# Performance work log

Hardware: AMD Instinct MI355X
Metric: run time of the kernel (lower is better)

Reference implementation:

```python
import jax, jax.numpy as jnp
import numpy as np

B, S, D = 16, 1024, 512
H, DH = 8, 64  # heads, dim_head


def setup_inputs() -> dict:
    key = jax.random.key(0)
    ks = jax.random.split(key, 7)
    x = jax.random.normal(ks[0], (B, S, D), dtype=jnp.float32)
    # variable sequence lengths in [1, S]
    seq_lens = jnp.maximum(jax.random.randint(ks[1], (B,), 0, S + 1), 1).astype(jnp.int32)
    w_std = 0.02
    Wq = jax.random.normal(ks[2], (D, D), dtype=jnp.float32) * w_std
    Wk = jax.random.normal(ks[3], (D, D), dtype=jnp.float32) * w_std
    Wv = jax.random.normal(ks[4], (D, D), dtype=jnp.float32) * w_std
    Wo = jax.random.normal(ks[5], (D, D), dtype=jnp.float32) * w_std
    bo = jnp.zeros((D,), dtype=jnp.float32)
    return {"x": x, "seq_lens": seq_lens, "Wq": Wq, "Wk": Wk, "Wv": Wv, "Wo": Wo, "bo": bo}


def reference(x, seq_lens, Wq, Wk, Wv, Wo, bo):
    # x: [B, S, D] padded ragged batch; seq_lens: [B] valid token counts.
    # Equivalent to the per-batch SDPA loop over jagged sequences: attention
    # is computed only among the valid tokens of each sequence.
    scale = DH ** -0.5
    q = (x @ Wq).reshape(B, S, H, DH)
    k = (x @ Wk).reshape(B, S, H, DH)
    v = (x @ Wv).reshape(B, S, H, DH)
    scores = jnp.einsum('bqhd,bkhd->bhqk', q, k) * scale  # [B,H,S,S]
    valid = jnp.arange(S)[None, :] < seq_lens[:, None]     # [B,S] token mask
    neg_inf = jnp.finfo(scores.dtype).min
    scores = jnp.where(valid[:, None, None, :], scores, neg_inf)
    attn = jax.nn.softmax(scores, axis=-1)
    out = jnp.einsum('bhqk,bkhd->bqhd', attn, v).reshape(B, S, D)
    out = out @ Wo + bo  # to_out Linear (dropout=0 / eval)
    return out * valid[:, :, None]  # zero padded query positions
```

## Files before the change

### kernel.cpp

```cpp
#include <hip/hip_runtime.h>
#include <hip/hip_bf16.h>

typedef __bf16 bf16_t;
typedef __attribute__((ext_vector_type(4))) __bf16 bf16x4;
typedef __attribute__((ext_vector_type(8))) __bf16 bf16x8;
typedef __attribute__((ext_vector_type(4))) float f32x4;

#define MFMA16(a, b, c) __builtin_amdgcn_mfma_f32_16x16x32_bf16((a), (b), (c), 0, 0, 0)

#define BB 16
#define SS 1024
#define DD 512
#define HH 8
#define DH 64
#define NTOK (BB * SS)
#define QSCALE 0.18033688f

typedef const __attribute__((address_space(1))) void gas_void;
typedef __attribute__((address_space(3))) void las_void;

__device__ __forceinline__ void async_cp16(const void* g, void* l) {
    __builtin_amdgcn_global_load_lds((gas_void*)g, (las_void*)l, 16, 0, 0);
}

__device__ __forceinline__ bf16x8 frag_ld(const char* sm, int row, int kk, int g) {
    int r7 = row & 7;
    int base = row * 128 + ((g & 1) << 3);
    int c0 = ((kk << 2) + (g >> 1)) ^ r7;
    int c1 = ((kk << 2) + 2 + (g >> 1)) ^ r7;
    bf16x4 lo = *(const bf16x4*)(sm + base + (c0 << 4));
    bf16x4 hi = *(const bf16x4*)(sm + base + (c1 << 4));
    return __builtin_shufflevector(lo, hi, 0, 1, 2, 3, 4, 5, 6, 7);
}

__global__ __launch_bounds__(256) void cast_x_k(const float* __restrict__ x,
                                                bf16_t* __restrict__ xb, int n4) {
    int i = blockIdx.x * 256 + threadIdx.x;
    if (i < n4) {
        float4 v = ((const float4*)x)[i];
        bf16x4 o;
        o[0] = (bf16_t)v.x; o[1] = (bf16_t)v.y; o[2] = (bf16_t)v.z; o[3] = (bf16_t)v.w;
        *(bf16x4*)(xb + (size_t)i * 4) = o;
    }
}

__global__ __launch_bounds__(256) void transpose_w_k(const float* __restrict__ W0,
                                                     const float* __restrict__ W1,
                                                     const float* __restrict__ W2,
                                                     const float* __restrict__ W3,
                                                     bf16_t* __restrict__ Wt) {
    __shared__ float t[32][33];
    int z = blockIdx.z;
    const float* W = (z == 0) ? W0 : (z == 1) ? W1 : (z == 2) ? W2 : W3;
    bf16_t* out = Wt + (size_t)z * DD * DD;
    int n0 = blockIdx.x * 32, k0 = blockIdx.y * 32;
    int tx = threadIdx.x, ty = threadIdx.y;
#pragma unroll
    for (int i = 0; i < 32; i += 8)
        t[ty + i][tx] = W[(size_t)(k0 + ty + i) * DD + n0 + tx];
    __syncthreads();
#pragma unroll
    for (int i = 0; i < 32; i += 8)
        out[(size_t)(n0 + ty + i) * DD + k0 + tx] = (bf16_t)t[tx][ty + i];
}

template <int MODE>
__global__ __launch_bounds__(256) void gemm_k(const bf16_t* __restrict__ A,
                                              const bf16_t* __restrict__ WtBase,
                                              bf16_t* __restrict__ oQ,
                                              bf16_t* __restrict__ oK,
                                              bf16_t* __restrict__ oVt,
                                              float* __restrict__ oO,
                                              const float* __restrict__ bo,
                                              const int* __restrict__ seq_lens) {
    __shared__ __align__(16) char smem[32768];
    char* smA = smem;
    char* smB = smem + 16384;
    const int tid = threadIdx.x;
    const int l = tid & 63, w = tid >> 6;
    const int lr = l & 15, g = l >> 4;
    const int bm = blockIdx.x, bn = blockIdx.y;
    const int z = (MODE == 0) ? blockIdx.z : 3;
    const bf16_t* Wt = WtBase + (size_t)z * DD * DD;
    const int row0 = bm * 128;
    const int col0 = bn * 128;
    const int wm = (w >> 1) * 64, wn = (w & 1) * 64;

    f32x4 acc[4][4] = {};

    for (int kt = 0; kt < 8; ++kt) {
        const int k0 = kt * 64;
        __syncthreads();
#pragma unroll
        for (int it = 0; it < 4; ++it) {
            int cl = it * 256 + tid;
            int m = cl >> 3, p = cl & 7, c = p ^ (m & 7);
            async_cp16(A + (size_t)(row0 + m) * DD + k0 + c * 8, smA + cl * 16);
        }
#pragma unroll
        for (int it = 0; it < 4; ++it) {
            int cl = it * 256 + tid;
            int m = cl >> 3, p = cl & 7, c = p ^ (m & 7);
            async_cp16(Wt + (size_t)(col0 + m) * DD + k0 + c * 8, smB + cl * 16);
        }
        __syncthreads();
#pragma unroll
        for (int kk = 0; kk < 2; ++kk) {
            bf16x8 af[4], bfr[4];
#pragma unroll
            for (int i = 0; i < 4; ++i) af[i] = frag_ld(smA, wm + i * 16 + lr, kk, g);
#pragma unroll
            for (int j = 0; j < 4; ++j) bfr[j] = frag_ld(smB, wn + j * 16 + lr, kk, g);
#pragma unroll
            for (int i = 0; i < 4; ++i)
#pragma unroll
                for (int j = 0; j < 4; ++j)
                    acc[i][j] = MFMA16(af[i], bfr[j], acc[i][j]);
        }
    }

    if (MODE == 0) {
        if (z < 2) {
            bf16_t* outp = (z == 0) ? oQ : oK;
            const float sc = (z == 0) ? QSCALE : 1.f;
#pragma unroll
            for (int i = 0; i < 4; ++i) {
                int mrow = row0 + wm + i * 16 + g * 4;
#pragma unroll
                for (int j = 0; j < 4; ++j) {
                    int n = col0 + wn + j * 16 + lr;
                    int h = n >> 6, dh = n & 63;
#pragma unroll
                    for (int r = 0; r < 4; ++r) {
                        int m = mrow + r;
                        int b = m >> 10, s = m & 1023;
                        outp[((size_t)((b * HH + h) * SS + s)) * DH + dh] =
                            (bf16_t)(acc[i][j][r] * sc);
                    }
                }
            }
        } else {
            __syncthreads();
            bf16_t* tsm = (bf16_t*)smem;
#pragma unroll
            for (int i = 0; i < 4; ++i)
#pragma unroll
                for (int j = 0; j < 4; ++j)
#pragma unroll
                    for (int r = 0; r < 4; ++r)
                        tsm[(wm + i * 16 + g * 4 + r) * 128 + wn + j * 16 + lr] =
                            (bf16_t)acc[i][j][r];
            __syncthreads();
            int nloc = tid >> 1;
            int mbase = (tid & 1) * 64;
            int n = col0 + nloc;
            int h = n >> 6, dh = n & 63;
            int b = row0 >> 10;
            int s0 = (row0 & 1023) + mbase;
            bf16_t* dst = oVt + ((size_t)((b * HH + h) * DH + dh)) * SS + s0;
#pragma unroll
            for (int mm = 0; mm < 64; mm += 8) {
                bf16x8 v;
#pragma unroll
                for (int e = 0; e < 8; ++e) v[e] = tsm[(mbase + mm + e) * 128 + nloc];
                *(bf16x8*)(dst + mm) = v;
            }
        }
    } else {
        int b = row0 >> 10;
        int len = seq_lens[b];
#pragma unroll
        for (int i = 0; i < 4; ++i) {
            int mrow = row0 + wm + i * 16 + g * 4;
#pragma unroll
            for (int j = 0; j < 4; ++j) {
                int n = col0 + wn + j * 16 + lr;
                float bias = bo[n];
#pragma unroll
                for (int r = 0; r < 4; ++r) {
                    int m = mrow + r;
                    int s = m & 1023;
                    oO[(size_t)m * DD + n] = (s < len) ? (acc[i][j][r] + bias) : 0.f;
                }
            }
        }
    }
}

__global__ __launch_bounds__(256) void attn_k(const bf16_t* __restrict__ Q,
                                              const bf16_t* __restrict__ K,
                                              const bf16_t* __restrict__ Vt,
                                              bf16_t* __restrict__ O,
                                              const int* __restrict__ seq_lens) {
    __shared__ __align__(16) char smem[32768];
    const int tid = threadIdx.x, l = tid & 63, w = tid >> 6;
    const int o = blockIdx.x;
    const int bh = ((o >> 6) << 3) | (o & 7);
    const int qt = (o >> 3) & 7;
    const int b = bh >> 3, h = bh & 7;
    const int len = seq_lens[b];
    const int q0 = qt * 128;
    if (q0 >= len) return;
    const int lr = l & 15, g = l >> 4;

    const bf16_t* kbase = K + (size_t)bh * SS * DH;
    const bf16_t* vbase = Vt + (size_t)bh * DH * SS;

    bf16x8 bq[2][2];
#pragma unroll
    for (int qs = 0; qs < 2; ++qs) {
        const bf16_t* qp = Q + ((size_t)bh * SS + q0 + w * 32 + qs * 16 + lr) * DH;
#pragma unroll
        for (int kk = 0; kk < 2; ++kk) {
            bf16x4 lo = *(const bf16x4*)(qp + kk * 32 + 4 * g);
            bf16x4 hi = *(const bf16x4*)(qp + kk * 32 + 16 + 4 * g);
            bq[qs][kk] = __builtin_shufflevector(lo, hi, 0, 1, 2, 3, 4, 5, 6, 7);
        }
    }

    f32x4 oacc[2][4] = {};
    float mrun[2] = {-1e30f, -1e30f};
    float lpart[2] = {0.f, 0.f};

    const int nkt = (len + 63) >> 6;

    auto stage = [&](int buf, int key0) {
        char* smK = smem + buf * 16384;
        char* smV = smK + 8192;
#pragma unroll
        for (int it = 0; it < 2; ++it) {
            int cl = it * 256 + tid;
            int m = cl >> 3, p = cl & 7, c = p ^ (m & 7);
            async_cp16(kbase + (size_t)(key0 + m) * DH + c * 8, smK + cl * 16);
        }
#pragma unroll
        for (int it = 0; it < 2; ++it) {
            int cl = it * 256 + tid;
            int m = cl >> 3, p = cl & 7, c = p ^ (m & 7);
            async_cp16(vbase + (size_t)m * SS + key0 + c * 8, smV + cl * 16);
        }
    };

    stage(0, 0);
    __syncthreads();

    for (int kt = 0; kt < nkt; ++kt) {
        const int key0 = kt * 64;
        const char* smK = smem + (kt & 1) * 16384;
        const char* smV = smK + 8192;
        if (kt + 1 < nkt) stage((kt + 1) & 1, key0 + 64);

        f32x4 pacc[2][4] = {};
#pragma unroll
        for (int nt = 0; nt < 4; ++nt) {
            bf16x8 ak0 = frag_ld(smK, nt * 16 + lr, 0, g);
            bf16x8 ak1 = frag_ld(smK, nt * 16 + lr, 1, g);
#pragma unroll
            for (int qs = 0; qs < 2; ++qs) {
                pacc[qs][nt] = MFMA16(ak0, bq[qs][0], pacc[qs][nt]);
                pacc[qs][nt] = MFMA16(ak1, bq[qs][1], pacc[qs][nt]);
            }
        }

        const bool full = (key0 + 64 <= len);

#pragma unroll
        for (int qs = 0; qs < 2; ++qs) {
            float mloc = -1e30f;
            if (full) {
#pragma unroll
                for (int nt = 0; nt < 4; ++nt)
#pragma unroll
                    for (int r = 0; r < 4; ++r) mloc = fmaxf(mloc, pacc[qs][nt][r]);
            } else {
#pragma unroll
                for (int nt = 0; nt < 4; ++nt)
#pragma unroll
                    for (int r = 0; r < 4; ++r) {
                        int kg = key0 + nt * 16 + 4 * g + r;
                        float s = (kg < len) ? pacc[qs][nt][r] : -1e30f;
                        pacc[qs][nt][r] = s;
                        mloc = fmaxf(mloc, s);
                    }
            }
            mloc = fmaxf(mloc, __shfl_xor(mloc, 16, 64));
            mloc = fmaxf(mloc, __shfl_xor(mloc, 32, 64));

            float mn;
            if (__all(mloc <= mrun[qs])) {
                mn = mrun[qs];
            } else {
                mn = fmaxf(mrun[qs], mloc);
                float corr = __builtin_amdgcn_exp2f(mrun[qs] - mn);
                mrun[qs] = mn;
                lpart[qs] *= corr;
                float cb[4];
#pragma unroll
                for (int r = 0; r < 4; ++r) cb[r] = __shfl(corr, 4 * g + r, 64);
#pragma unroll
                for (int dt = 0; dt < 4; ++dt)
#pragma unroll
                    for (int r = 0; r < 4; ++r) oacc[qs][dt][r] *= cb[r];
            }

            float ls = 0.f;
#pragma unroll
            for (int nt = 0; nt < 4; ++nt)
#pragma unroll
                for (int r = 0; r < 4; ++r) {
                    float p = __builtin_amdgcn_exp2f(pacc[qs][nt][r] - mn);
                    pacc[qs][nt][r] = p;
                    ls += p;
                }
            lpart[qs] += ls;

            bf16x8 pa[2];
#pragma unroll
            for (int kf = 0; kf < 2; ++kf)
#pragma unroll
                for (int j = 0; j < 8; ++j)
                    pa[kf][j] = (bf16_t)pacc[qs][2 * kf + (j >> 2)][j & 3];
#pragma unroll
            for (int kf = 0; kf < 2; ++kf)
#pragma unroll
                for (int dt = 0; dt < 4; ++dt) {
                    bf16x8 bv = frag_ld(smV, dt * 16 + lr, kf, g);
                    oacc[qs][dt] = MFMA16(pa[kf], bv, oacc[qs][dt]);
                }
        }
        __syncthreads();
    }

#pragma unroll
    for (int qs = 0; qs < 2; ++qs) {
        float lt = lpart[qs];
        lt += __shfl_xor(lt, 16, 64);
        lt += __shfl_xor(lt, 32, 64);
#pragma unroll
        for (int r = 0; r < 4; ++r) {
            float inv = 1.f / __shfl(lt, 4 * g + r, 64);
            int q = q0 + w * 32 + qs * 16 + 4 * g + r;
            size_t orow = ((size_t)b * SS + q) * DD;
#pragma unroll
            for (int dt = 0; dt < 4; ++dt)
                O[orow + h * DH + dt * 16 + lr] = (bf16_t)(oacc[qs][dt][r] * inv);
        }
    }
}

extern "C" void kernel_launch(void* const* d_in, const int* in_sizes, int n_in,
                              void* d_out, int out_size, void* d_ws, size_t ws_size,
                              hipStream_t stream) {
    const float* x = (const float*)d_in[0];
    const int* seq_lens = (const int*)d_in[1];
    const float* Wq = (const float*)d_in[2];
    const float* Wk = (const float*)d_in[3];
    const float* Wv = (const float*)d_in[4];
    const float* Wo = (const float*)d_in[5];
    const float* bo = (const float*)d_in[6];
    float* out = (float*)d_out;

    char* ws = (char*)d_ws;
    const size_t SEG = (size_t)NTOK * DD * sizeof(bf16_t);
    bf16_t* xb = (bf16_t*)ws;
    bf16_t* qb = (bf16_t*)(ws + SEG);
    bf16_t* kb = (bf16_t*)(ws + 2 * SEG);
    bf16_t* vtb = (bf16_t*)(ws + 3 * SEG);
    bf16_t* wt = (bf16_t*)(ws + 4 * SEG);
    bf16_t* ab = xb;

    cast_x_k<<<dim3((NTOK * DD / 4) / 256), dim3(256), 0, stream>>>(x, xb, NTOK * DD / 4);
    transpose_w_k<<<dim3(16, 16, 4), dim3(32, 8), 0, stream>>>(Wq, Wk, Wv, Wo, wt);
    gemm_k<0><<<dim3(NTOK / 128, DD / 128, 3), dim3(256), 0, stream>>>(
        xb, wt, qb, kb, vtb, nullptr, nullptr, nullptr);
    attn_k<<<dim3(BB * HH * (SS / 128)), dim3(256), 0, stream>>>(qb, kb, vtb, ab, seq_lens);
    gemm_k<2><<<dim3(NTOK / 128, DD / 128, 1), dim3(256), 0, stream>>>(
        ab, wt, nullptr, nullptr, nullptr, out, bo, seq_lens);
}
```

Measured before the change: 129.8 us.

## Use persistent attention blocks with atomic work queue sorted by sequence length

Adds a tiny kernel that sorts batches by sequence length (longest first) and builds a list of valid (batch, head, query-tile) work items. The attention kernel becomes persistent, with 512 blocks pulling items from an atomic cursor, so no blocks are launched for empty tiles and long items start first for better load balance. It also precomputes the swizzled LDS fragment offsets once instead of per load. The cost is an extra launch, a serialized atomic plus barrier per item, and fixed assumptions about grid size and workspace layout.

```diff
diff --git a/kernel.cpp b/kernel.cpp
--- a/kernel.cpp
+++ b/kernel.cpp
@@ -30,6 +30,12 @@
     int c1 = ((kk << 2) + 2 + (g >> 1)) ^ r7;
     bf16x4 lo = *(const bf16x4*)(sm + base + (c0 << 4));
     bf16x4 hi = *(const bf16x4*)(sm + base + (c1 << 4));
+    return __builtin_shufflevector(lo, hi, 0, 1, 2, 3, 4, 5, 6, 7);
+}
+
+__device__ __forceinline__ bf16x8 frag_at(const char* smrow, int a0, int a1) {
+    bf16x4 lo = *(const bf16x4*)(smrow + a0);
+    bf16x4 hi = *(const bf16x4*)(smrow + a1);
     return __builtin_shufflevector(lo, hi, 0, 1, 2, 3, 4, 5, 6, 7);
 }
 
@@ -62,6 +68,37 @@
 #pragma unroll
     for (int i = 0; i < 32; i += 8)
         out[(size_t)(n0 + ty + i) * DD + k0 + tx] = (bf16_t)t[tx][ty + i];
+}
+
+__global__ void build_q_k(const int* __restrict__ sl, ushort* __restrict__ items,
+                          int* __restrict__ meta) {
+    int l = threadIdx.x;
+    __shared__ int s_b[BB], s_cnt[BB], s_start[BB];
+    if (l < BB) {
+        int len = sl[l];
+        int rank = 0;
+        for (int j = 0; j < BB; ++j) {
+            int lj = sl[j];
+            if (lj > len || (lj == len && j < l)) ++rank;
+        }
+        s_b[rank] = l;
+        s_cnt[rank] = ((len + 127) >> 7) * HH;
+    }
+    __syncthreads();
+    if (l < BB) {
+        int st = 0;
+        for (int j = 0; j < l; ++j) st += s_cnt[j];
+        s_start[l] = st;
+        if (l == BB - 1) { meta[0] = st + s_cnt[l]; meta[1] = 0; }
+    }
+    __syncthreads();
+    if (l < BB) {
+        int b = s_b[l], st = s_start[l], c = s_cnt[l];
+        for (int i = 0; i < c; ++i) {
+            int qt = i >> 3, h = i & 7;
+            items[st + i] = (ushort)((((b << 3) | h) << 3) | qt);
+        }
+    }
 }
 
 template <int MODE>
@@ -191,159 +228,178 @@
                                               const bf16_t* __restrict__ K,
                                               const bf16_t* __restrict__ Vt,
                                               bf16_t* __restrict__ O,
-                                              const int* __restrict__ seq_lens) {
+                                              const int* __restrict__ seq_lens,
+                                              const ushort* __restrict__ items,
+                                              int* __restrict__ meta) {
     __shared__ __align__(16) char smem[32768];
+    __shared__ int s_item;
     const int tid = threadIdx.x, l = tid & 63, w = tid >> 6;
-    const int o = blockIdx.x;
-    const int bh = ((o >> 6) << 3) | (o & 7);
-    const int qt = (o >> 3) & 7;
-    const int b = bh >> 3, h = bh & 7;
-    const int len = seq_lens[b];
-    const int q0 = qt * 128;
-    if (q0 >= len) return;
     const int lr = l & 15, g = l >> 4;
-
-    const bf16_t* kbase = K + (size_t)bh * SS * DH;
-    const bf16_t* vbase = Vt + (size_t)bh * DH * SS;
-
-    bf16x8 bq[2][2];
-#pragma unroll
-    for (int qs = 0; qs < 2; ++qs) {
-        const bf16_t* qp = Q + ((size_t)bh * SS + q0 + w * 32 + qs * 16 + lr) * DH;
-#pragma unroll
-        for (int kk = 0; kk < 2; ++kk) {
-            bf16x4 lo = *(const bf16x4*)(qp + kk * 32 + 4 * g);
-            bf16x4 hi = *(const bf16x4*)(qp + kk * 32 + 16 + 4 * g);
-            bq[qs][kk] = __builtin_shufflevector(lo, hi, 0, 1, 2, 3, 4, 5, 6, 7);
-        }
-    }
-
-    f32x4 oacc[2][4] = {};
-    float mrun[2] = {-1e30f, -1e30f};
-    float lpart[2] = {0.f, 0.f};
-
-    const int nkt = (len + 63) >> 6;
-
-    auto stage = [&](int buf, int key0) {
-        char* smK = smem + buf * 16384;
-        char* smV = smK + 8192;
-#pragma unroll
-        for (int it = 0; it < 2; ++it) {
-            int cl = it * 256 + tid;
-            int m = cl >> 3, p = cl & 7, c = p ^ (m & 7);
-            async_cp16(kbase + (size_t)(key0 + m) * DH + c * 8, smK + cl * 16);
-        }
-#pragma unroll
-        for (int it = 0; it < 2; ++it) {
-            int cl = it * 256 + tid;
-            int m = cl >> 3, p = cl & 7, c = p ^ (m & 7);
-            async_cp16(vbase + (size_t)m * SS + key0 + c * 8, smV + cl * 16);
-        }
-    };
-
-    stage(0, 0);
-    __syncthreads();
-
-    for (int kt = 0; kt < nkt; ++kt) {
-        const int key0 = kt * 64;
-        const char* smK = smem + (kt & 1) * 16384;
-        const char* smV = smK + 8192;
-        if (kt + 1 < nkt) stage((kt + 1) & 1, key0 + 64);
-
-        f32x4 pacc[2][4] = {};
-#pragma unroll
-        for (int nt = 0; nt < 4; ++nt) {
-            bf16x8 ak0 = frag_ld(smK, nt * 16 + lr, 0, g);
-            bf16x8 ak1 = frag_ld(smK, nt * 16 + lr, 1, g);
+    const int nitems = meta[0];
+    int* cursor = meta + 1;
+
+    const int x0 = lr * 128 + ((g & 1) << 3);
+    const int xr = lr & 7;
+    const int a00 = x0 + ((((g >> 1) + 0) ^ xr) << 4);
+    const int a01 = x0 + ((((g >> 1) + 2) ^ xr) << 4);
+    const int a10 = x0 + ((((g >> 1) + 4) ^ xr) << 4);
+    const int a11 = x0 + ((((g >> 1) + 6) ^ xr) << 4);
+
+    for (;;) {
+        if (tid == 0) s_item = atomicAdd(cursor, 1);
+        __syncthreads();
+        const int ii = s_item;
+        if (ii >= nitems) return;
+        const int itv = items[ii];
+        const int qt = itv & 7, bh = itv >> 3;
+        const int b = bh >> 3;
+        const int len = seq_lens[b];
+        const int q0 = qt * 128;
+        const int h = bh & 7;
+
+        const bf16_t* kbase = K + (size_t)bh * SS * DH;
+        const bf16_t* vbase = Vt + (size_t)bh * DH * SS;
+
+        bf16x8 bq[2][2];
+#pragma unroll
+        for (int qs = 0; qs < 2; ++qs) {
+            const bf16_t* qp = Q + ((size_t)bh * SS + q0 + w * 32 + qs * 16 + lr) * DH;
+#pragma unroll
+            for (int kk = 0; kk < 2; ++kk) {
+                bf16x4 lo = *(const bf16x4*)(qp + kk * 32 + 4 * g);
+                bf16x4 hi = *(const bf16x4*)(qp + kk * 32 + 16 + 4 * g);
+                bq[qs][kk] = __builtin_shufflevector(lo, hi, 0, 1, 2, 3, 4, 5, 6, 7);
+            }
+        }
+
+        f32x4 oacc[2][4] = {};
+        float mrun[2] = {-1e30f, -1e30f};
+        float lpart[2] = {0.f, 0.f};
+
+        const int nkt = (len + 63) >> 6;
+
+        auto stage = [&](int buf, int key0) {
+            char* smK = smem + buf * 16384;
+            char* smV = smK + 8192;
+#pragma unroll
+            for (int it = 0; it < 2; ++it) {
+                int cl = it * 256 + tid;
+                int m = cl >> 3, p = cl & 7, c = p ^ (m & 7);
+                async_cp16(kbase + (size_t)(key0 + m) * DH + c * 8, smK + cl * 16);
+            }
+#pragma unroll
+            for (int it = 0; it < 2; ++it) {
+                int cl = it * 256 + tid;
+                int m = cl >> 3, p = cl & 7, c = p ^ (m & 7);
+                async_cp16(vbase + (size_t)m * SS + key0 + c * 8, smV + cl * 16);
+            }
+        };
+
+        stage(0, 0);
+        __syncthreads();
+
+        for (int kt = 0; kt < nkt; ++kt) {
+            const int key0 = kt * 64;
+            const char* smK = smem + (kt & 1) * 16384;
+            const char* smV = smK + 8192;
+            if (kt + 1 < nkt) stage((kt + 1) & 1, key0 + 64);
+
+            f32x4 pacc[2][4] = {};
+#pragma unroll
+            for (int nt = 0; nt < 4; ++nt) {
+                bf16x8 ak0 = frag_at(smK + nt * 2048, a00, a01);
+                bf16x8 ak1 = frag_at(smK + nt * 2048, a10, a11);
+#pragma unroll
+                for (int qs = 0; qs < 2; ++qs) {
+                    pacc[qs][nt] = MFMA16(ak0, bq[qs][0], pacc[qs][nt]);
+                    pacc[qs][nt] = MFMA16(ak1, bq[qs][1], pacc[qs][nt]);
+                }
+            }
+
+            const bool full = (key0 + 64 <= len);
+
 #pragma unroll
             for (int qs = 0; qs < 2; ++qs) {
-                pacc[qs][nt] = MFMA16(ak0, bq[qs][0], pacc[qs][nt]);
-                pacc[qs][nt] = MFMA16(ak1, bq[qs][1], pacc[qs][nt]);
-            }
-        }
-
-        const bool full = (key0 + 64 <= len);
+                float mloc = -1e30f;
+                if (full) {
+#pragma unroll
+                    for (int nt = 0; nt < 4; ++nt)
+#pragma unroll
+                        for (int r = 0; r < 4; ++r) mloc = fmaxf(mloc, pacc[qs][nt][r]);
+                } else {
+#pragma unroll
+                    for (int nt = 0; nt < 4; ++nt)
+#pragma unroll
+                        for (int r = 0; r < 4; ++r) {
+                            int kg = key0 + nt * 16 + 4 * g + r;
+                            float s = (kg < len) ? pacc[qs][nt][r] : -1e30f;
+                            pacc[qs][nt][r] = s;
+                            mloc = fmaxf(mloc, s);
+                        }
+                }
+                mloc = fmaxf(mloc, __shfl_xor(mloc, 16, 64));
+                mloc = fmaxf(mloc, __shfl_xor(mloc, 32, 64));
+
+                float mn;
+                if (__all(mloc <= mrun[qs])) {
+                    mn = mrun[qs];
+                } else {
+                    mn = fmaxf(mrun[qs], mloc);
+                    float corr = __builtin_amdgcn_exp2f(mrun[qs] - mn);
+                    mrun[qs] = mn;
+                    lpart[qs] *= corr;
+                    float cb[4];
+#pragma unroll
+                    for (int r = 0; r < 4; ++r) cb[r] = __shfl(corr, 4 * g + r, 64);
+#pragma unroll
+                    for (int dt = 0; dt < 4; ++dt)
+#pragma unroll
+                        for (int r = 0; r < 4; ++r) oacc[qs][dt][r] *= cb[r];
+                }
+
+                float ls = 0.f;
+#pragma unroll
+                for (int nt = 0; nt < 4; ++nt)
+#pragma unroll
+                    for (int r = 0; r < 4; ++r) {
+                        float p = __builtin_amdgcn_exp2f(pacc[qs][nt][r] - mn);
+                        pacc[qs][nt][r] = p;
+                        ls += p;
+                    }
+                lpart[qs] += ls;
+
+                bf16x8 pa[2];
+#pragma unroll
+                for (int kf = 0; kf < 2; ++kf)
+#pragma unroll
+                    for (int j = 0; j < 8; ++j)
+                        pa[kf][j] = (bf16_t)pacc[qs][2 * kf + (j >> 2)][j & 3];
+#pragma unroll
+                for (int kf = 0; kf < 2; ++kf)
+#pragma unroll
+                    for (int dt = 0; dt < 4; ++dt) {
+                        bf16x8 bv = frag_at(smV + dt * 2048, kf ? a10 : a00,
+                                            kf ? a11 : a01);
+                        oacc[qs][dt] = MFMA16(pa[kf], bv, oacc[qs][dt]);
+                    }
+            }
+            __syncthreads();
+        }
 
 #pragma unroll
         for (int qs = 0; qs < 2; ++qs) {
-            float mloc = -1e30f;
-            if (full) {
-#pragma unroll
-                for (int nt = 0; nt < 4; ++nt)
-#pragma unroll
-                    for (int r = 0; r < 4; ++r) mloc = fmaxf(mloc, pacc[qs][nt][r]);
-            } else {
-#pragma unroll
-                for (int nt = 0; nt < 4; ++nt)
-#pragma unroll
-                    for (int r = 0; r < 4; ++r) {
-                        int kg = key0 + nt * 16 + 4 * g + r;
-                        float s = (kg < len) ? pacc[qs][nt][r] : -1e30f;
-                        pacc[qs][nt][r] = s;
-                        mloc = fmaxf(mloc, s);
-                    }
-            }
-            mloc = fmaxf(mloc, __shfl_xor(mloc, 16, 64));
-            mloc = fmaxf(mloc, __shfl_xor(mloc, 32, 64));
-
-            float mn;
-            if (__all(mloc <= mrun[qs])) {
-                mn = mrun[qs];
-            } else {
-                mn = fmaxf(mrun[qs], mloc);
-                float corr = __builtin_amdgcn_exp2f(mrun[qs] - mn);
-                mrun[qs] = mn;
-                lpart[qs] *= corr;
-                float cb[4];
-#pragma unroll
-                for (int r = 0; r < 4; ++r) cb[r] = __shfl(corr, 4 * g + r, 64);
+            float lt = lpart[qs];
+            lt += __shfl_xor(lt, 16, 64);
+            lt += __shfl_xor(lt, 32, 64);
+#pragma unroll
+            for (int r = 0; r < 4; ++r) {
+                float inv = 1.f / __shfl(lt, 4 * g + r, 64);
+                int q = q0 + w * 32 + qs * 16 + 4 * g + r;
+                size_t orow = ((size_t)b * SS + q) * DD;
 #pragma unroll
                 for (int dt = 0; dt < 4; ++dt)
-#pragma unroll
-                    for (int r = 0; r < 4; ++r) oacc[qs][dt][r] *= cb[r];
-            }
-
-            float ls = 0.f;
-#pragma unroll
-            for (int nt = 0; nt < 4; ++nt)
-#pragma unroll
-                for (int r = 0; r < 4; ++r) {
-                    float p = __builtin_amdgcn_exp2f(pacc[qs][nt][r] - mn);
-                    pacc[qs][nt][r] = p;
-                    ls += p;
-                }
-            lpart[qs] += ls;
-
-            bf16x8 pa[2];
-#pragma unroll
-            for (int kf = 0; kf < 2; ++kf)
-#pragma unroll
-                for (int j = 0; j < 8; ++j)
-                    pa[kf][j] = (bf16_t)pacc[qs][2 * kf + (j >> 2)][j & 3];
-#pragma unroll
-            for (int kf = 0; kf < 2; ++kf)
-#pragma unroll
-                for (int dt = 0; dt < 4; ++dt) {
-                    bf16x8 bv = frag_ld(smV, dt * 16 + lr, kf, g);
-                    oacc[qs][dt] = MFMA16(pa[kf], bv, oacc[qs][dt]);
-                }
-        }
-        __syncthreads();
-    }
-
-#pragma unroll
-    for (int qs = 0; qs < 2; ++qs) {
-        float lt = lpart[qs];
-        lt += __shfl_xor(lt, 16, 64);
-        lt += __shfl_xor(lt, 32, 64);
-#pragma unroll
-        for (int r = 0; r < 4; ++r) {
-            float inv = 1.f / __shfl(lt, 4 * g + r, 64);
-            int q = q0 + w * 32 + qs * 16 + 4 * g + r;
-            size_t orow = ((size_t)b * SS + q) * DD;
-#pragma unroll
-            for (int dt = 0; dt < 4; ++dt)
-                O[orow + h * DH + dt * 16 + lr] = (bf16_t)(oacc[qs][dt][r] * inv);
+                    O[orow + h * DH + dt * 16 + lr] = (bf16_t)(oacc[qs][dt][r] * inv);
+            }
         }
     }
 }
@@ -367,13 +423,16 @@
     bf16_t* kb = (bf16_t*)(ws + 2 * SEG);
     bf16_t* vtb = (bf16_t*)(ws + 3 * SEG);
     bf16_t* wt = (bf16_t*)(ws + 4 * SEG);
+    ushort* items = (ushort*)(ws + 4 * SEG + (size_t)4 * DD * DD * sizeof(bf16_t));
+    int* meta = (int*)(items + 1024);
     bf16_t* ab = xb;
 
+    build_q_k<<<dim3(1), dim3(64), 0, stream>>>(seq_lens, items, meta);
     cast_x_k<<<dim3((NTOK * DD / 4) / 256), dim3(256), 0, stream>>>(x, xb, NTOK * DD / 4);
     transpose_w_k<<<dim3(16, 16, 4), dim3(32, 8), 0, stream>>>(Wq, Wk, Wv, Wo, wt);
     gemm_k<0><<<dim3(NTOK / 128, DD / 128, 3), dim3(256), 0, stream>>>(
         xb, wt, qb, kb, vtb, nullptr, nullptr, nullptr);
-    attn_k<<<dim3(BB * HH * (SS / 128)), dim3(256), 0, stream>>>(qb, kb, vtb, ab, seq_lens);
+    attn_k<<<dim3(512), dim3(256), 0, stream>>>(qb, kb, vtb, ab, seq_lens, items, meta);
     gemm_k<2><<<dim3(NTOK / 128, DD / 128, 1), dim3(256), 0, stream>>>(
         ab, wt, nullptr, nullptr, nullptr, out, bo, seq_lens);
 }
```

Result: slower. 134.7 us (+3.8%).
